# Performance work log

Measured on AMD Instinct MI355X. Metric: run time of the kernel, lower is better.

## Reference

```python
import jax, jax.numpy as jnp
import numpy as np

N, S, C = 2048, 14, 30  # batch, grid, channels (B=2 boxes*5 + 20 classes)
L_COORD, L_NOOBJ = 5.0, 0.5


def setup_inputs() -> dict:
    key = jax.random.key(0)
    k1, k2, k3 = jax.random.split(key, 3)
    pred = jax.random.uniform(k1, (N, S, S, C), minval=0.05, maxval=1.0, dtype=jnp.float32)
    target = jax.random.uniform(k2, (N, S, S, C), minval=0.05, maxval=1.0, dtype=jnp.float32)
    conf = (jax.random.uniform(k3, (N, S, S)) > 0.7).astype(jnp.float32)
    target = target.at[..., 4].set(conf)
    return {"pred": pred, "target": target}


def _to_xyxy(b):
    # b[..., :2] = center (grid units, divided by 14), b[..., 2:4] = w,h (image units)
    xy = b[..., :2] / 14.0
    wh = b[..., 2:4]
    return jnp.concatenate([xy - 0.5 * wh, xy + 0.5 * wh], axis=-1)


def _yolo_loss(pred, target):
    n = pred.shape[0]
    coo = (target[..., 4] > 0).astype(pred.dtype)   # [N,S,S] object mask
    noo = 1.0 - coo                                  # no-object mask
    pb = pred[..., :10].reshape(pred.shape[:3] + (2, 5))    # [N,S,S,2,5]
    tb = target[..., :10].reshape(target.shape[:3] + (2, 5))

    # IoU of the 2 predicted boxes vs the FIRST target box of the cell
    p_xy = _to_xyxy(pb)              # [N,S,S,2,4]
    t_xy = _to_xyxy(tb[..., 0, :])   # [N,S,S,4]
    lt = jnp.maximum(p_xy[..., :2], t_xy[..., None, :2])
    rb = jnp.minimum(p_xy[..., 2:], t_xy[..., None, 2:])
    wh = jnp.clip(rb - lt, 0.0)
    inter = wh[..., 0] * wh[..., 1]                          # [N,S,S,2]
    a1 = (p_xy[..., 2] - p_xy[..., 0]) * (p_xy[..., 3] - p_xy[..., 1])
    a2 = ((t_xy[..., 2] - t_xy[..., 0]) * (t_xy[..., 3] - t_xy[..., 1]))[..., None]
    iou = inter / (a1 + a2 - inter)

    # responsible box = argmax IoU (selection only; IoU value never enters the
    # loss because the original writes max_iou into cols :4 but reads col 4=0)
    r = jnp.argmax(jax.lax.stop_gradient(iou), axis=-1)      # [N,S,S]
    idx = r[..., None, None]
    resp_p = jnp.take_along_axis(pb, idx, axis=3)[..., 0, :]      # [N,S,S,5]
    resp_t = jnp.take_along_axis(tb, idx, axis=3)[..., 0, :]
    nresp_p = jnp.take_along_axis(pb, 1 - idx, axis=3)[..., 0, :]

    cm = coo[..., None]
    loc = jnp.sum(cm * (resp_p[..., :2] - resp_t[..., :2]) ** 2) \
        + jnp.sum(cm * (jnp.sqrt(resp_p[..., 2:4]) - jnp.sqrt(resp_t[..., 2:4])) ** 2)
    contain = jnp.sum(coo * resp_p[..., 4] ** 2)       # target IoU col 4 is 0 in original
    not_contain = jnp.sum(coo * nresp_p[..., 4] ** 2)  # target conf zeroed in original
    noobj = jnp.sum(noo * ((pred[..., 4] - target[..., 4]) ** 2
                           + (pred[..., 9] - target[..., 9]) ** 2))
    cls = jnp.sum(cm * (pred[..., 10:] - target[..., 10:]) ** 2)
    return (L_COORD * loc + 2.0 * contain + not_contain + L_NOOBJ * noobj + cls) / n


def reference(pred, target):
    return _yolo_loss(pred, target)
```

## Files before the change

### kernel.cpp

```cpp
#include <hip/hip_runtime.h>


constexpr int N_IMG  = 2048;
constexpr int NC     = 30;
constexpr int CELLS  = N_IMG * 14 * 14;
constexpr int BLOCK  = 256;
constexpr int CPB    = 256;
constexpr int NCHUNK = 7;
constexpr int GRID   = CELLS / (CPB * NCHUNK);
constexpr float INV14 = 1.0f / 14.0f;

__device__ __forceinline__ void gload16(const void* g, void* l) {
    __builtin_amdgcn_global_load_lds(
        (const __attribute__((address_space(1))) void*)g,
        (__attribute__((address_space(3))) void*)l, 16, 0, 0);
}

__device__ __forceinline__ float cell_loss(const float* __restrict__ cp,
                                           const float* __restrict__ ct)
{
    float pv[NC], tv[NC];
    const float2* p2 = reinterpret_cast<const float2*>(cp);
    const float2* t2 = reinterpret_cast<const float2*>(ct);
    #pragma unroll
    for (int i = 0; i < NC / 2; ++i) {
        float2 a = p2[i]; pv[2*i] = a.x; pv[2*i+1] = a.y;
        float2 b = t2[i]; tv[2*i] = b.x; tv[2*i+1] = b.y;
    }

    const float coo = (tv[4] > 0.0f) ? 1.0f : 0.0f;

    const float txc = tv[0] * INV14, tyc = tv[1] * INV14;
    const float tx1 = txc - 0.5f * tv[2], ty1 = tyc - 0.5f * tv[3];
    const float tx2 = txc + 0.5f * tv[2], ty2 = tyc + 0.5f * tv[3];
    const float t_area = (tx2 - tx1) * (ty2 - ty1);

    float i0, u0;
    {
        const float xc = pv[0] * INV14, yc = pv[1] * INV14;
        const float x1 = xc - 0.5f * pv[2], y1 = yc - 0.5f * pv[3];
        const float x2 = xc + 0.5f * pv[2], y2 = yc + 0.5f * pv[3];
        const float a1 = (x2 - x1) * (y2 - y1);
        const float wx = fmaxf(fminf(x2, tx2) - fmaxf(x1, tx1), 0.0f);
        const float wy = fmaxf(fminf(y2, ty2) - fmaxf(y1, ty1), 0.0f);
        i0 = wx * wy;
        u0 = a1 + t_area - i0;
    }
    float i1, u1;
    {
        const float xc = pv[5] * INV14, yc = pv[6] * INV14;
        const float x1 = xc - 0.5f * pv[7], y1 = yc - 0.5f * pv[8];
        const float x2 = xc + 0.5f * pv[7], y2 = yc + 0.5f * pv[8];
        const float a1 = (x2 - x1) * (y2 - y1);
        const float wx = fmaxf(fminf(x2, tx2) - fmaxf(x1, tx1), 0.0f);
        const float wy = fmaxf(fminf(y2, ty2) - fmaxf(y1, ty1), 0.0f);
        i1 = wx * wy;
        u1 = a1 + t_area - i1;
    }

    const bool sel = (i1 * u0) > (i0 * u1);
    const float rp0 = sel ? pv[5] : pv[0];
    const float rp1 = sel ? pv[6] : pv[1];
    const float rp2 = sel ? pv[7] : pv[2];
    const float rp3 = sel ? pv[8] : pv[3];
    const float rp4 = sel ? pv[9] : pv[4];
    const float rt0 = sel ? tv[5] : tv[0];
    const float rt1 = sel ? tv[6] : tv[1];
    const float rt2 = sel ? tv[7] : tv[2];
    const float rt3 = sel ? tv[8] : tv[3];
    const float nrp4 = sel ? pv[4] : pv[9];

    const float d0 = rp0 - rt0, d1 = rp1 - rt1;
    const float d2 = sqrtf(rp2) - sqrtf(rt2);
    const float d3 = sqrtf(rp3) - sqrtf(rt3);
    const float loc     = d0*d0 + d1*d1 + d2*d2 + d3*d3;
    const float contain = rp4 * rp4;
    const float notc    = nrp4 * nrp4;
    const float e4 = pv[4] - tv[4], e9 = pv[9] - tv[9];
    const float noobj = e4*e4 + e9*e9;
    float cls = 0.0f;
    #pragma unroll
    for (int c = 10; c < NC; ++c) { const float d = pv[c] - tv[c]; cls += d*d; }

    return coo * (5.0f * loc + 2.0f * contain + notc + cls)
         + (1.0f - coo) * (0.5f * noobj);
}

__global__ __launch_bounds__(BLOCK)
void yolo_main(const float* __restrict__ pred,
               const float* __restrict__ targ,
               float* __restrict__ partial)
{
    __shared__ float sp[2][CPB * NC];
    __shared__ float st[2][CPB * NC];

    const int tid = threadIdx.x;
    const int bid = blockIdx.x;

    auto stage = [&](int buf, int c) {
        const size_t fbase = (size_t)(bid * NCHUNK + c) * (size_t)(CPB * NC);
        const float4* gp = reinterpret_cast<const float4*>(pred + fbase);
        const float4* gt = reinterpret_cast<const float4*>(targ + fbase);
        float4* lp = reinterpret_cast<float4*>(sp[buf]);
        float4* lt = reinterpret_cast<float4*>(st[buf]);
        #pragma unroll
        for (int i = 0; i < 7; ++i)
            gload16(gp + i * BLOCK + tid, lp + i * BLOCK + tid);
        if (tid < 128)
            gload16(gp + 7 * BLOCK + tid, lp + 7 * BLOCK + tid);
        #pragma unroll
        for (int i = 0; i < 7; ++i)
            gload16(gt + i * BLOCK + tid, lt + i * BLOCK + tid);
        if (tid < 128)
            gload16(gt + 7 * BLOCK + tid, lt + 7 * BLOCK + tid);
    };

    stage(0, 0);
    __syncthreads();

    float acc = 0.0f;
    for (int c = 0; c < NCHUNK; ++c) {
        const int cur = c & 1;
        if (c + 1 < NCHUNK) stage(cur ^ 1, c + 1);
        acc += cell_loss(&sp[cur][tid * NC], &st[cur][tid * NC]);
        __syncthreads();
    }

    __shared__ float wsum[BLOCK / 64];
    #pragma unroll
    for (int o = 32; o > 0; o >>= 1) acc += __shfl_down(acc, o, 64);
    if ((tid & 63) == 0) wsum[tid >> 6] = acc;
    __syncthreads();
    if (tid == 0)
        partial[bid] = wsum[0] + wsum[1] + wsum[2] + wsum[3];
}

__global__ __launch_bounds__(64)
void yolo_final(const float* __restrict__ partial, float* __restrict__ out)
{
    const int tid = threadIdx.x;
    double s = 0.0;
    for (int i = tid; i < GRID; i += 64) s += (double)partial[i];
    #pragma unroll
    for (int o = 32; o > 0; o >>= 1) s += __shfl_down(s, o, 64);
    if (tid == 0) out[0] = (float)(s / (double)N_IMG);
}

extern "C" void kernel_launch(void* const* d_in, const int* in_sizes, int n_in,
                              void* d_out, int out_size, void* d_ws, size_t ws_size,
                              hipStream_t stream)
{
    const float* pred = (const float*)d_in[0];
    const float* targ = (const float*)d_in[1];
    float* out        = (float*)d_out;
    float* partial    = (float*)d_ws;

    yolo_main<<<GRID, BLOCK, 0, stream>>>(pred, targ, partial);
    yolo_final<<<1, 64, 0, stream>>>(partial, out);
}
```

Measured before the change: 24.20 us.

## Fuse final reduction via atomics, use grid-stride chunks and split cell work across threads

Replaces the two-kernel reduction with a single fused kernel that atomically adds each block's scaled partial sum into the output, after a memset. Chunks shrink to 128 cells and a fixed grid of 512 blocks walks them grid-stride with double-buffered LDS loads. Each cell's work is split between two threads: one computes box/IoU/confidence terms, the other the 20-channel class term, which lowers per-thread register pressure. Float atomics make the summation order nondeterministic, and the memset adds a small extra operation.

```diff
diff --git a/kernel.cpp b/kernel.cpp
--- a/kernel.cpp
+++ b/kernel.cpp
@@ -5,10 +5,11 @@
 constexpr int NC     = 30;
 constexpr int CELLS  = N_IMG * 14 * 14;
 constexpr int BLOCK  = 256;
-constexpr int CPB    = 256;
-constexpr int NCHUNK = 7;
-constexpr int GRID   = CELLS / (CPB * NCHUNK);
+constexpr int CPB    = 128;
+constexpr int NCHUNK = CELLS / CPB;
+constexpr int GRID   = 512;
 constexpr float INV14 = 1.0f / 14.0f;
+constexpr float INVN  = 1.0f / (float)N_IMG;
 
 __device__ __forceinline__ void gload16(const void* g, void* l) {
     __builtin_amdgcn_global_load_lds(
@@ -16,134 +17,136 @@
         (__attribute__((address_space(3))) void*)l, 16, 0, 0);
 }
 
-__device__ __forceinline__ float cell_loss(const float* __restrict__ cp,
-                                           const float* __restrict__ ct)
-{
-    float pv[NC], tv[NC];
-    const float2* p2 = reinterpret_cast<const float2*>(cp);
-    const float2* t2 = reinterpret_cast<const float2*>(ct);
-    #pragma unroll
-    for (int i = 0; i < NC / 2; ++i) {
-        float2 a = p2[i]; pv[2*i] = a.x; pv[2*i+1] = a.y;
-        float2 b = t2[i]; tv[2*i] = b.x; tv[2*i+1] = b.y;
-    }
-
-    const float coo = (tv[4] > 0.0f) ? 1.0f : 0.0f;
-
-    const float txc = tv[0] * INV14, tyc = tv[1] * INV14;
-    const float tx1 = txc - 0.5f * tv[2], ty1 = tyc - 0.5f * tv[3];
-    const float tx2 = txc + 0.5f * tv[2], ty2 = tyc + 0.5f * tv[3];
-    const float t_area = (tx2 - tx1) * (ty2 - ty1);
-
-    float i0, u0;
-    {
-        const float xc = pv[0] * INV14, yc = pv[1] * INV14;
-        const float x1 = xc - 0.5f * pv[2], y1 = yc - 0.5f * pv[3];
-        const float x2 = xc + 0.5f * pv[2], y2 = yc + 0.5f * pv[3];
-        const float a1 = (x2 - x1) * (y2 - y1);
-        const float wx = fmaxf(fminf(x2, tx2) - fmaxf(x1, tx1), 0.0f);
-        const float wy = fmaxf(fminf(y2, ty2) - fmaxf(y1, ty1), 0.0f);
-        i0 = wx * wy;
-        u0 = a1 + t_area - i0;
-    }
-    float i1, u1;
-    {
-        const float xc = pv[5] * INV14, yc = pv[6] * INV14;
-        const float x1 = xc - 0.5f * pv[7], y1 = yc - 0.5f * pv[8];
-        const float x2 = xc + 0.5f * pv[7], y2 = yc + 0.5f * pv[8];
-        const float a1 = (x2 - x1) * (y2 - y1);
-        const float wx = fmaxf(fminf(x2, tx2) - fmaxf(x1, tx1), 0.0f);
-        const float wy = fmaxf(fminf(y2, ty2) - fmaxf(y1, ty1), 0.0f);
-        i1 = wx * wy;
-        u1 = a1 + t_area - i1;
-    }
-
-    const bool sel = (i1 * u0) > (i0 * u1);
-    const float rp0 = sel ? pv[5] : pv[0];
-    const float rp1 = sel ? pv[6] : pv[1];
-    const float rp2 = sel ? pv[7] : pv[2];
-    const float rp3 = sel ? pv[8] : pv[3];
-    const float rp4 = sel ? pv[9] : pv[4];
-    const float rt0 = sel ? tv[5] : tv[0];
-    const float rt1 = sel ? tv[6] : tv[1];
-    const float rt2 = sel ? tv[7] : tv[2];
-    const float rt3 = sel ? tv[8] : tv[3];
-    const float nrp4 = sel ? pv[4] : pv[9];
-
-    const float d0 = rp0 - rt0, d1 = rp1 - rt1;
-    const float d2 = sqrtf(rp2) - sqrtf(rt2);
-    const float d3 = sqrtf(rp3) - sqrtf(rt3);
-    const float loc     = d0*d0 + d1*d1 + d2*d2 + d3*d3;
-    const float contain = rp4 * rp4;
-    const float notc    = nrp4 * nrp4;
-    const float e4 = pv[4] - tv[4], e9 = pv[9] - tv[9];
-    const float noobj = e4*e4 + e9*e9;
-    float cls = 0.0f;
-    #pragma unroll
-    for (int c = 10; c < NC; ++c) { const float d = pv[c] - tv[c]; cls += d*d; }
-
-    return coo * (5.0f * loc + 2.0f * contain + notc + cls)
-         + (1.0f - coo) * (0.5f * noobj);
-}
-
 __global__ __launch_bounds__(BLOCK)
-void yolo_main(const float* __restrict__ pred,
-               const float* __restrict__ targ,
-               float* __restrict__ partial)
+void yolo_fused(const float* __restrict__ pred,
+                const float* __restrict__ targ,
+                float* __restrict__ out)
 {
     __shared__ float sp[2][CPB * NC];
     __shared__ float st[2][CPB * NC];
+    __shared__ float wsum[BLOCK / 64];
 
     const int tid = threadIdx.x;
     const int bid = blockIdx.x;
 
     auto stage = [&](int buf, int c) {
-        const size_t fbase = (size_t)(bid * NCHUNK + c) * (size_t)(CPB * NC);
+        const size_t fbase = (size_t)c * (size_t)(CPB * NC);
         const float4* gp = reinterpret_cast<const float4*>(pred + fbase);
         const float4* gt = reinterpret_cast<const float4*>(targ + fbase);
         float4* lp = reinterpret_cast<float4*>(sp[buf]);
         float4* lt = reinterpret_cast<float4*>(st[buf]);
         #pragma unroll
-        for (int i = 0; i < 7; ++i)
+        for (int i = 0; i < 3; ++i)
             gload16(gp + i * BLOCK + tid, lp + i * BLOCK + tid);
-        if (tid < 128)
-            gload16(gp + 7 * BLOCK + tid, lp + 7 * BLOCK + tid);
+        if (tid < 192)
+            gload16(gp + 3 * BLOCK + tid, lp + 3 * BLOCK + tid);
         #pragma unroll
-        for (int i = 0; i < 7; ++i)
+        for (int i = 0; i < 3; ++i)
             gload16(gt + i * BLOCK + tid, lt + i * BLOCK + tid);
-        if (tid < 128)
-            gload16(gt + 7 * BLOCK + tid, lt + 7 * BLOCK + tid);
+        if (tid < 192)
+            gload16(gt + 3 * BLOCK + tid, lt + 3 * BLOCK + tid);
     };
 
-    stage(0, 0);
+    float acc = 0.0f;
+    stage(0, bid);
     __syncthreads();
 
-    float acc = 0.0f;
-    for (int c = 0; c < NCHUNK; ++c) {
-        const int cur = c & 1;
-        if (c + 1 < NCHUNK) stage(cur ^ 1, c + 1);
-        acc += cell_loss(&sp[cur][tid * NC], &st[cur][tid * NC]);
+    int it = 0;
+    for (int c = bid; c < NCHUNK; c += GRID, ++it) {
+        const int buf = it & 1;
+        if (c + GRID < NCHUNK) stage(buf ^ 1, c + GRID);
+
+        if (tid < CPB) {
+            const float* cp = &sp[buf][tid * NC];
+            const float* ct = &st[buf][tid * NC];
+            float pv[10], tv[10];
+            const float2* p2 = reinterpret_cast<const float2*>(cp);
+            const float2* t2 = reinterpret_cast<const float2*>(ct);
+            #pragma unroll
+            for (int i = 0; i < 5; ++i) {
+                float2 a = p2[i]; pv[2*i] = a.x; pv[2*i+1] = a.y;
+                float2 b = t2[i]; tv[2*i] = b.x; tv[2*i+1] = b.y;
+            }
+
+            const float coo = (tv[4] > 0.0f) ? 1.0f : 0.0f;
+
+            const float txc = tv[0] * INV14, tyc = tv[1] * INV14;
+            const float tx1 = txc - 0.5f * tv[2], ty1 = tyc - 0.5f * tv[3];
+            const float tx2 = txc + 0.5f * tv[2], ty2 = tyc + 0.5f * tv[3];
+            const float t_area = (tx2 - tx1) * (ty2 - ty1);
+
+            float i0, u0;
+            {
+                const float xc = pv[0] * INV14, yc = pv[1] * INV14;
+                const float x1 = xc - 0.5f * pv[2], y1 = yc - 0.5f * pv[3];
+                const float x2 = xc + 0.5f * pv[2], y2 = yc + 0.5f * pv[3];
+                const float a1 = (x2 - x1) * (y2 - y1);
+                const float wx = fmaxf(fminf(x2, tx2) - fmaxf(x1, tx1), 0.0f);
+                const float wy = fmaxf(fminf(y2, ty2) - fmaxf(y1, ty1), 0.0f);
+                i0 = wx * wy;
+                u0 = a1 + t_area - i0;
+            }
+            float i1, u1;
+            {
+                const float xc = pv[5] * INV14, yc = pv[6] * INV14;
+                const float x1 = xc - 0.5f * pv[7], y1 = yc - 0.5f * pv[8];
+                const float x2 = xc + 0.5f * pv[7], y2 = yc + 0.5f * pv[8];
+                const float a1 = (x2 - x1) * (y2 - y1);
+                const float wx = fmaxf(fminf(x2, tx2) - fmaxf(x1, tx1), 0.0f);
+                const float wy = fmaxf(fminf(y2, ty2) - fmaxf(y1, ty1), 0.0f);
+                i1 = wx * wy;
+                u1 = a1 + t_area - i1;
+            }
+
+            const bool sel = (i1 * u0) > (i0 * u1);
+            const float rp0 = sel ? pv[5] : pv[0];
+            const float rp1 = sel ? pv[6] : pv[1];
+            const float rp2 = sel ? pv[7] : pv[2];
+            const float rp3 = sel ? pv[8] : pv[3];
+            const float rp4 = sel ? pv[9] : pv[4];
+            const float rt0 = sel ? tv[5] : tv[0];
+            const float rt1 = sel ? tv[6] : tv[1];
+            const float rt2 = sel ? tv[7] : tv[2];
+            const float rt3 = sel ? tv[8] : tv[3];
+            const float nrp4 = sel ? pv[4] : pv[9];
+
+            const float d0 = rp0 - rt0, d1 = rp1 - rt1;
+            const float d2 = sqrtf(rp2) - sqrtf(rt2);
+            const float d3 = sqrtf(rp3) - sqrtf(rt3);
+            const float loc     = d0*d0 + d1*d1 + d2*d2 + d3*d3;
+            const float contain = rp4 * rp4;
+            const float notc    = nrp4 * nrp4;
+            const float e4 = pv[4] - tv[4], e9 = pv[9] - tv[9];
+            const float noobj = e4*e4 + e9*e9;
+
+            acc += coo * (5.0f * loc + 2.0f * contain + notc)
+                 + (1.0f - coo) * (0.5f * noobj);
+        } else {
+            const int cell = tid - CPB;
+            const float* cp = &sp[buf][cell * NC];
+            const float* ct = &st[buf][cell * NC];
+            const float coo = (ct[4] > 0.0f) ? 1.0f : 0.0f;
+            float cls = 0.0f;
+            const float2* p2 = reinterpret_cast<const float2*>(cp + 10);
+            const float2* t2 = reinterpret_cast<const float2*>(ct + 10);
+            #pragma unroll
+            for (int i = 0; i < 10; ++i) {
+                float2 a = p2[i];
+                float2 b = t2[i];
+                const float dx = a.x - b.x, dy = a.y - b.y;
+                cls += dx * dx + dy * dy;
+            }
+            acc += coo * cls;
+        }
         __syncthreads();
     }
 
-    __shared__ float wsum[BLOCK / 64];
     #pragma unroll
     for (int o = 32; o > 0; o >>= 1) acc += __shfl_down(acc, o, 64);
     if ((tid & 63) == 0) wsum[tid >> 6] = acc;
     __syncthreads();
     if (tid == 0)
-        partial[bid] = wsum[0] + wsum[1] + wsum[2] + wsum[3];
-}
-
-__global__ __launch_bounds__(64)
-void yolo_final(const float* __restrict__ partial, float* __restrict__ out)
-{
-    const int tid = threadIdx.x;
-    double s = 0.0;
-    for (int i = tid; i < GRID; i += 64) s += (double)partial[i];
-    #pragma unroll
-    for (int o = 32; o > 0; o >>= 1) s += __shfl_down(s, o, 64);
-    if (tid == 0) out[0] = (float)(s / (double)N_IMG);
+        atomicAdd(out, (wsum[0] + wsum[1] + wsum[2] + wsum[3]) * INVN);
 }
 
 extern "C" void kernel_launch(void* const* d_in, const int* in_sizes, int n_in,
@@ -153,8 +156,7 @@
     const float* pred = (const float*)d_in[0];
     const float* targ = (const float*)d_in[1];
     float* out        = (float*)d_out;
-    float* partial    = (float*)d_ws;
 
-    yolo_main<<<GRID, BLOCK, 0, stream>>>(pred, targ, partial);
-    yolo_final<<<1, 64, 0, stream>>>(partial, out);
+    hipMemsetAsync(out, 0, sizeof(float), stream);
+    yolo_fused<<<GRID, BLOCK, 0, stream>>>(pred, targ, out);
 }
```

New measurement: 28.88 us. 1.19x slower.

## Use grid-stride triple-buffered 64-cell chunks with wave-specialized async loads

Applied to the files above, without the earlier changes.

Replaces the 224-block, 7-chunk double-buffered scheme with a 768-block grid-stride loop over 64-cell chunks. Each of the four waves stages a quarter of the chunk into a triple-buffered LDS ring: two waves load pred and two load target. Only the first wave computes the loss. Explicit vmcnt waits and raw s_barrier replace __syncthreads so two chunks stay in flight. The aim is more blocks in flight to better saturate memory bandwidth, at the cost of idle compute lanes and hand-tuned wait counts that must match the number of issued loads.

```diff
diff --git a/kernel.cpp b/kernel.cpp
--- a/kernel.cpp
+++ b/kernel.cpp
@@ -5,10 +5,15 @@
 constexpr int NC     = 30;
 constexpr int CELLS  = N_IMG * 14 * 14;
 constexpr int BLOCK  = 256;
-constexpr int CPB    = 256;
-constexpr int NCHUNK = 7;
-constexpr int GRID   = CELLS / (CPB * NCHUNK);
+constexpr int CPB    = 64;
+constexpr int NCHT   = CELLS / CPB;
+constexpr int GRID   = 768;
 constexpr float INV14 = 1.0f / 14.0f;
+
+constexpr int FPB   = 2 * CPB * NC;
+constexpr int SLOTS = FPB / 4;
+constexpr int SPW   = SLOTS / 4;
+constexpr int PREDS = CPB * NC / 4;
 
 __device__ __forceinline__ void gload16(const void* g, void* l) {
     __builtin_amdgcn_global_load_lds(
@@ -91,39 +96,51 @@
                const float* __restrict__ targ,
                float* __restrict__ partial)
 {
-    __shared__ float sp[2][CPB * NC];
-    __shared__ float st[2][CPB * NC];
+    __shared__ float sbuf[3 * FPB];
 
     const int tid = threadIdx.x;
     const int bid = blockIdx.x;
+    const int wv  = tid >> 6;
+    const int ln  = tid & 63;
 
-    auto stage = [&](int buf, int c) {
-        const size_t fbase = (size_t)(bid * NCHUNK + c) * (size_t)(CPB * NC);
-        const float4* gp = reinterpret_cast<const float4*>(pred + fbase);
-        const float4* gt = reinterpret_cast<const float4*>(targ + fbase);
-        float4* lp = reinterpret_cast<float4*>(sp[buf]);
-        float4* lt = reinterpret_cast<float4*>(st[buf]);
+    auto stage = [&](float* lbuf, int chunk) {
+        const size_t fbase = (size_t)chunk * (size_t)(CPB * NC);
+        const int wbase = wv * SPW;
+        const float4* gsrc = (wv < 2)
+            ? reinterpret_cast<const float4*>(pred + fbase) + wbase
+            : reinterpret_cast<const float4*>(targ + fbase) + (wbase - PREDS);
+        float4* lb = reinterpret_cast<float4*>(lbuf) + wbase;
         #pragma unroll
-        for (int i = 0; i < 7; ++i)
-            gload16(gp + i * BLOCK + tid, lp + i * BLOCK + tid);
-        if (tid < 128)
-            gload16(gp + 7 * BLOCK + tid, lp + 7 * BLOCK + tid);
-        #pragma unroll
-        for (int i = 0; i < 7; ++i)
-            gload16(gt + i * BLOCK + tid, lt + i * BLOCK + tid);
-        if (tid < 128)
-            gload16(gt + 7 * BLOCK + tid, lt + 7 * BLOCK + tid);
+        for (int i = 0; i < 3; ++i)
+            gload16(gsrc + i * 64 + ln, lb + i * 64 + ln);
+        if (ln < 48)
+            gload16(gsrc + 192 + ln, lb + 192 + ln);
     };
 
-    stage(0, 0);
-    __syncthreads();
+    const int n = (NCHT - bid + GRID - 1) / GRID;
+
+    stage(sbuf, bid);
+    stage(sbuf + FPB, bid + GRID);
+    asm volatile("s_waitcnt vmcnt(4)" ::: "memory");
+    __builtin_amdgcn_sched_barrier(0);
+    __builtin_amdgcn_s_barrier();
+    __builtin_amdgcn_sched_barrier(0);
 
     float acc = 0.0f;
-    for (int c = 0; c < NCHUNK; ++c) {
-        const int cur = c & 1;
-        if (c + 1 < NCHUNK) stage(cur ^ 1, c + 1);
-        acc += cell_loss(&sp[cur][tid * NC], &st[cur][tid * NC]);
-        __syncthreads();
+    for (int k = 0; k < n; ++k) {
+        const bool pre = (k + 2 < n);
+        if (pre) stage(sbuf + ((k + 2) % 3) * FPB, bid + (k + 2) * GRID);
+
+        if (tid < CPB) {
+            const float* b = sbuf + (k % 3) * FPB;
+            acc += cell_loss(b + tid * NC, b + CPB * NC + tid * NC);
+        }
+
+        if (pre) asm volatile("s_waitcnt vmcnt(4)" ::: "memory");
+        else     asm volatile("s_waitcnt vmcnt(0)" ::: "memory");
+        __builtin_amdgcn_sched_barrier(0);
+        __builtin_amdgcn_s_barrier();
+        __builtin_amdgcn_sched_barrier(0);
     }
 
     __shared__ float wsum[BLOCK / 64];
@@ -140,7 +157,8 @@
 {
     const int tid = threadIdx.x;
     double s = 0.0;
-    for (int i = tid; i < GRID; i += 64) s += (double)partial[i];
+    #pragma unroll
+    for (int i = 0; i < GRID / 64; ++i) s += (double)partial[tid + i * 64];
     #pragma unroll
     for (int o = 32; o > 0; o >>= 1) s += __shfl_down(s, o, 64);
     if (tid == 0) out[0] = (float)(s / (double)N_IMG);
```

Result: faster. 22.67 us, median of 2 (-6.3%).
